# Performance work log

Hardware: AMD Instinct MI355X
Metric: run time of the kernel (lower is better)

The kernel has to match this reference:

```python
import jax, jax.numpy as jnp
import numpy as np
import math

B, N, CS, CZ, H, C, P, PV, NB = 1, 512, 384, 128, 12, 16, 4, 8, 64


def quat_to_rot(q):
    q = q / jnp.clip(jnp.linalg.norm(q, axis=-1, keepdims=True), 1e-8)
    w, x, y, z = q[..., 0], q[..., 1], q[..., 2], q[..., 3]
    return jnp.stack([
        w*w + x*x - y*y - z*z, 2*(x*y - w*z), 2*(x*z + w*y),
        2*(x*y + w*z), w*w - x*x + y*y - z*z, 2*(y*z - w*x),
        2*(x*z - w*y), 2*(y*z + w*x), w*w - x*x - y*y + z*z,
    ], axis=-1).reshape(q.shape[:-1] + (3, 3))


def setup_inputs() -> dict:
    key = jax.random.key(0)
    ks = jax.random.split(key, 28)
    def n(k, shape, sc=1.0):
        return jax.random.normal(k, shape, jnp.float32) * sc
    s = n(ks[0], (B, N, CS))
    z = n(ks[1], (B, N, N, CZ))
    translations = n(ks[2], (B, N, 3)) * 4.0  # spread distances over 0-32A bins
    rotations = quat_to_rot(n(ks[3], (B, N, 4)))  # valid SO(3) frames
    mask = jnp.ones((B, N), dtype=bool)
    inv = lambda fan: 1.0 / math.sqrt(fan)
    return {
        's': s, 'z': z, 'translations': translations, 'rotations': rotations, 'mask': mask,
        'Wq': n(ks[4], (CS, H*C), inv(CS)), 'bq': n(ks[5], (H*C,), 0.01),
        'Wk': n(ks[6], (CS, H*C), inv(CS)), 'bk': n(ks[7], (H*C,), 0.01),
        'Wv': n(ks[8], (CS, H*C), inv(CS)), 'bv': n(ks[9], (H*C,), 0.01),
        'Wqp': n(ks[10], (CS, H*P*3), inv(CS)), 'bqp': n(ks[11], (H*P*3,), 0.01),
        'Wkp': n(ks[12], (CS, H*P*3), inv(CS)), 'bkp': n(ks[13], (H*P*3,), 0.01),
        'Wvp': n(ks[14], (CS, H*PV*3), inv(CS)), 'bvp': n(ks[15], (H*PV*3,), 0.01),
        'Wb': n(ks[16], (CZ, H), inv(CZ)), 'bb': n(ks[17], (H,), 0.01),
        'dist_emb': n(ks[18], (NB, H), 0.02),
        'scale_logits': n(ks[19], (3, H), 0.1),
        'head_weights': jnp.abs(n(ks[20], (H,))) * 0.2 + 0.8,
        'Wout': n(ks[21], (H*(C + PV*4 + CZ), CS), inv(H*(C + PV*4 + CZ))),
        'bout': n(ks[22], (CS,), 0.01),
    }


def reference(s, z, translations, rotations, mask, Wq, bq, Wk, bk, Wv, bv,
              Wqp, bqp, Wkp, bkp, Wvp, bvp, Wb, bb, dist_emb, scale_logits,
              head_weights, Wout, bout):
    b, n, _ = s.shape
    q = (s @ Wq + bq).reshape(b, n, H, C)
    k = (s @ Wk + bk).reshape(b, n, H, C)
    v = (s @ Wv + bv).reshape(b, n, H, C)
    q_pts = (s @ Wqp + bqp).reshape(b, n, H, P, 3)
    k_pts = (s @ Wkp + bkp).reshape(b, n, H, P, 3)
    v_pts = (s @ Wvp + bvp).reshape(b, n, H, PV, 3)
    t = translations[:, :, None, None, :]
    q_g = jnp.einsum('bnij,bnhpj->bnhpi', rotations, q_pts) + t
    k_g = jnp.einsum('bnij,bnhpj->bnhpi', rotations, k_pts) + t
    v_g = jnp.einsum('bnij,bnhpj->bnhpi', rotations, v_pts) + t
    scalar_logits = jnp.einsum('bnhc,bmhc->bnmh', q, k) / math.sqrt(C)
    # squared point distances, summed over points p and coords i, via expansion
    q_sq = (q_g**2).sum((-1, -2))  # (b, n, h)
    k_sq = (k_g**2).sum((-1, -2))
    cross = jnp.einsum('bnhpi,bmhpi->bnmh', q_g, k_g)
    point_dist = q_sq[:, :, None, :] + k_sq[:, None, :, :] - 2.0 * cross
    point_logits = -0.5 * point_dist * head_weights
    pair_bias = z @ Wb + bb  # (b, n, m, h)
    pair_dist = jnp.linalg.norm(
        translations[:, :, None, :] - translations[:, None, :, :], axis=-1)
    edges = jnp.linspace(0.0, 32.0, NB + 1)
    bins = jnp.clip(jnp.searchsorted(edges, pair_dist, side='left') - 1, 0, NB - 1)
    dist_bias = dist_emb[bins]
    local = (pair_dist <= 5.0).astype(s.dtype)
    medium = ((pair_dist > 5.0) & (pair_dist <= 15.0)).astype(s.dtype)
    scales = jnp.stack([local, medium, jnp.ones_like(pair_dist)], axis=-1)
    per_head = jax.nn.softmax(scale_logits, axis=0)  # (3, h)
    multiscale = jnp.einsum('bnms,sh->bnmh', scales, per_head)
    logits = scalar_logits + point_logits + pair_bias + dist_bias + multiscale
    m2d = mask[:, :, None] & mask[:, None, :]
    logits = jnp.where(m2d[..., None], logits, -10000.0)
    attn = jax.nn.softmax(logits.astype(jnp.float32), axis=2).astype(s.dtype)
    out_scalar = jnp.einsum('bnmh,bmhc->bnhc', attn, v)
    out_pts_g = jnp.einsum('bnmh,bmhpi->bnhpi', attn, v_g)
    out_pts_l = jnp.einsum('bnji,bnhpj->bnhpi', rotations, out_pts_g - t)  # R^T x
    out_norms = jnp.linalg.norm(out_pts_l, axis=-1)  # (b, n, h, pv)
    pair_feat = jnp.einsum('bnmh,bnmc->bnhc', attn, z)
    feats = jnp.concatenate(
        [out_scalar, out_pts_l.reshape(b, n, H, PV * 3), out_norms, pair_feat],
        axis=-1).reshape(b, n, -1)
    return feats @ Wout + bout
```

## Files before the change

### kernel.cpp

```cpp
#include <hip/hip_runtime.h>
#include <math.h>

#define N   512
#define CS  384
#define CZ  128
#define H   12
#define C   16
#define P   4
#define PV  8
#define NB  64
#define KSP 528
#define QKD 28
#define QPAD 68
#define APAD 516

#define OFF_Q    0
#define OFF_K    98304
#define OFF_V    196608
#define OFF_QP   294912
#define OFF_KP   368640
#define OFF_VP   442368
#define OFF_QG   589824
#define OFF_KG   663552
#define OFF_VG   737280
#define OFF_QSQ  884736
#define OFF_KSQ  890880
#define OFF_LOG  897024
#define OFF_FEAT 4042752

__global__ __launch_bounds__(256) void k_proj(
    const float* __restrict__ s,
    const float* __restrict__ Wq,  const float* __restrict__ bq,
    const float* __restrict__ Wk,  const float* __restrict__ bk,
    const float* __restrict__ Wv,  const float* __restrict__ bv,
    const float* __restrict__ Wqp, const float* __restrict__ bqp,
    const float* __restrict__ Wkp, const float* __restrict__ bkp,
    const float* __restrict__ Wvp, const float* __restrict__ bvp,
    float* __restrict__ ws)
{
    __shared__ float s_s[16*388];
    __shared__ float part[4*16*68];
    const int tid = threadIdx.x;
    const int n0  = blockIdx.y * 16;
    const int cq  = tid & 15;
    const int rg  = (tid >> 4) & 3;
    const int ks  = tid >> 6;
    const int gc  = blockIdx.x * 64 + cq * 4;
    for (int i = tid; i < 16*384; i += 256) {
        int r = i / 384, c = i - r*384;
        s_s[r*388 + c] = s[(n0 + r)*384 + c];
    }
    __syncthreads();
    const float* W; int width; int lc;
    if      (gc < 192) { W=Wq;  width=192; lc=gc;     }
    else if (gc < 384) { W=Wk;  width=192; lc=gc-192; }
    else if (gc < 576) { W=Wv;  width=192; lc=gc-384; }
    else if (gc < 720) { W=Wqp; width=144; lc=gc-576; }
    else if (gc < 864) { W=Wkp; width=144; lc=gc-720; }
    else               { W=Wvp; width=288; lc=gc-864; }
    float acc[4][4] = {{0.f}};
    const float* wp   = W + lc + (size_t)(ks*96)*width;
    const float* srow = s_s + (rg*4)*388 + ks*96;
    #pragma unroll 4
    for (int kk = 0; kk < 96; kk++) {
        float4 w4 = *(const float4*)(wp + (size_t)kk*width);
        #pragma unroll
        for (int r = 0; r < 4; r++) {
            float sv = srow[r*388 + kk];
            acc[r][0] += sv*w4.x; acc[r][1] += sv*w4.y;
            acc[r][2] += sv*w4.z; acc[r][3] += sv*w4.w;
        }
    }
    #pragma unroll
    for (int r = 0; r < 4; r++)
        *(float4*)(part + (ks*16 + rg*4 + r)*68 + cq*4) =
            make_float4(acc[r][0], acc[r][1], acc[r][2], acc[r][3]);
    __syncthreads();
    {
        const int row = tid >> 4;
        float4 sum = *(const float4*)(part + (0*16 + row)*68 + cq*4);
        #pragma unroll
        for (int k2 = 1; k2 < 4; k2++) {
            float4 p = *(const float4*)(part + (k2*16 + row)*68 + cq*4);
            sum.x += p.x; sum.y += p.y; sum.z += p.z; sum.w += p.w;
        }
        const float* b; float* dst; int w2, lc2;
        if      (gc < 192) { b=bq;  w2=192; lc2=gc;     dst=ws+OFF_Q;  }
        else if (gc < 384) { b=bk;  w2=192; lc2=gc-192; dst=ws+OFF_K;  }
        else if (gc < 576) { b=bv;  w2=192; lc2=gc-384; dst=ws+OFF_V;  }
        else if (gc < 720) { b=bqp; w2=144; lc2=gc-576; dst=ws+OFF_QP; }
        else if (gc < 864) { b=bkp; w2=144; lc2=gc-720; dst=ws+OFF_KP; }
        else               { b=bvp; w2=288; lc2=gc-864; dst=ws+OFF_VP; }
        float4 b4 = *(const float4*)(b + lc2);
        sum.x += b4.x; sum.y += b4.y; sum.z += b4.z; sum.w += b4.w;
        *(float4*)(dst + (size_t)(n0+row)*w2 + lc2) = sum;
    }
}

__global__ __launch_bounds__(192) void k_frames(
    const float* __restrict__ rot, const float* __restrict__ trans,
    float* __restrict__ ws)
{
    int n = blockIdx.x, tid = threadIdx.x;
    __shared__ float R[9], T[3], qg_s[144], kg_s[144];
    if (tid < 9) R[tid] = rot[n*9 + tid];
    if (tid < 3) T[tid] = trans[n*3 + tid];
    __syncthreads();
    if (tid < 48) {
        const float* lp = ws + OFF_QP + n*144 + tid*3;
        float l0=lp[0], l1=lp[1], l2=lp[2];
        float* gp = ws + OFF_QG + n*144 + tid*3;
        for (int i=0;i<3;i++){ float g = R[i*3+0]*l0 + R[i*3+1]*l1 + R[i*3+2]*l2 + T[i]; gp[i]=g; qg_s[tid*3+i]=g; }
    } else if (tid < 96) {
        int u = tid-48;
        const float* lp = ws + OFF_KP + n*144 + u*3;
        float l0=lp[0], l1=lp[1], l2=lp[2];
        float* gp = ws + OFF_KG + n*144 + u*3;
        for (int i=0;i<3;i++){ float g = R[i*3+0]*l0 + R[i*3+1]*l1 + R[i*3+2]*l2 + T[i]; gp[i]=g; kg_s[u*3+i]=g; }
    } else {
        int u = tid-96;
        const float* lp = ws + OFF_VP + n*288 + u*3;
        float l0=lp[0], l1=lp[1], l2=lp[2];
        float* gp = ws + OFF_VG + n*288 + u*3;
        for (int i=0;i<3;i++){ float g = R[i*3+0]*l0 + R[i*3+1]*l1 + R[i*3+2]*l2 + T[i]; gp[i]=g; }
    }
    __syncthreads();
    if (tid < 12) {
        float a=0;
        for (int d=0; d<12; d++){ float x=qg_s[tid*12+d]; a+=x*x; }
        ws[OFF_QSQ + n*12 + tid]=a;
    } else if (tid < 24) {
        int h = tid-12; float a=0;
        for (int d=0; d<12; d++){ float x=kg_s[h*12+d]; a+=x*x; }
        ws[OFF_KSQ + n*12 + h]=a;
    }
}

__global__ __launch_bounds__(256) void k_qkpt(
    const float* __restrict__ head_weights, float* __restrict__ ws)
{
    __shared__ float qs[QKD*QPAD], ks[QKD*QPAD], qa[64], kb[64];
    const int tid = threadIdx.x;
    const int m0 = blockIdx.x * 64, n0 = blockIdx.y * 64, h = blockIdx.z;
    const float hw = head_weights[h];
    for (int idx = tid; idx < 64*16; idx += 256) {
        int r = idx >> 4, c = idx & 15;
        qs[c*QPAD + r] = ws[OFF_Q + (n0+r)*192 + h*16 + c] * 0.25f;
        ks[c*QPAD + r] = ws[OFF_K + (m0+r)*192 + h*16 + c];
    }
    for (int idx = tid; idx < 64*12; idx += 256) {
        int r = idx / 12, c = idx % 12;
        qs[(16+c)*QPAD + r] = ws[OFF_QG + (n0+r)*144 + h*12 + c] * hw;
        ks[(16+c)*QPAD + r] = ws[OFF_KG + (m0+r)*144 + h*12 + c];
    }
    for (int idx = tid; idx < 64; idx += 256) {
        qa[idx] = -0.5f * hw * ws[OFF_QSQ + (n0+idx)*12 + h];
        kb[idx] = -0.5f * hw * ws[OFF_KSQ + (m0+idx)*12 + h];
    }
    __syncthreads();
    const int tx = tid & 15, ty = tid >> 4;
    float acc[4][4] = {{0.f}};
    #pragma unroll 4
    for (int d = 0; d < QKD; d++) {
        float4 a = *(const float4*)(qs + d*QPAD + ty*4);
        float4 b = *(const float4*)(ks + d*QPAD + tx*4);
        const float* ap = &a.x; const float* bp = &b.x;
        #pragma unroll
        for (int i=0;i<4;i++)
            #pragma unroll
            for (int j=0;j<4;j++) acc[i][j] += ap[i]*bp[j];
    }
    #pragma unroll
    for (int i=0;i<4;i++) {
        float ai = qa[ty*4+i];
        float4 r;
        r.x = acc[i][0] + ai + kb[tx*4+0];
        r.y = acc[i][1] + ai + kb[tx*4+1];
        r.z = acc[i][2] + ai + kb[tx*4+2];
        r.w = acc[i][3] + ai + kb[tx*4+3];
        *(float4*)(ws + OFF_LOG + ((size_t)(n0+ty*4+i)*H + h)*N + m0 + tx*4) = r;
    }
}

__global__ __launch_bounds__(256) void k_attn_all(
    const float* __restrict__ z, const float* __restrict__ trans,
    const float* __restrict__ rot,
    const float* __restrict__ Wb, const float* __restrict__ bb,
    const float* __restrict__ dist_emb, const float* __restrict__ scale_logits,
    float* __restrict__ ws)
{
    __shared__ float attn_s[H*APAD];
    __shared__ float part[4*12*64];
    __shared__ float og_s[288];
    const int n = blockIdx.x, tid = threadIdx.x;
    const int lane = tid & 63, wave = tid >> 6;

    const float4* asrc = (const float4*)(ws + OFF_LOG + (size_t)n*H*N);
    for (int i = tid; i < H*(N/4); i += 256) {
        int h = i >> 7, q = i & 127;
        *(float4*)(attn_s + h*APAD + q*4) = asrc[h*128 + q];
    }
    __syncthreads();

    const float tnx = trans[n*3+0], tny = trans[n*3+1], tnz = trans[n*3+2];
    for (int half = 0; half < 2; half++) {
        const int m = tid + half*256;
        float dx = tnx - trans[m*3+0];
        float dy = tny - trans[m*3+1];
        float dz = tnz - trans[m*3+2];
        float pd = sqrtf(dx*dx+dy*dy+dz*dz);
        int bin = (int)ceilf(2.f*pd) - 1;
        bin = bin < 0 ? 0 : (bin > NB-1 ? NB-1 : bin);
        const float4 de0 = *(const float4*)(dist_emb + bin*12);
        const float4 de1 = *(const float4*)(dist_emb + bin*12 + 4);
        const float4 de2 = *(const float4*)(dist_emb + bin*12 + 8);
        float de[12] = {de0.x,de0.y,de0.z,de0.w, de1.x,de1.y,de1.z,de1.w, de2.x,de2.y,de2.z,de2.w};
        float acc[12];
        #pragma unroll
        for (int h=0; h<12; h++) {
            float sa = scale_logits[0*H+h], sb = scale_logits[1*H+h], sc = scale_logits[2*H+h];
            float mx = fmaxf(sa, fmaxf(sb,sc));
            float ea=__expf(sa-mx), eb=__expf(sb-mx), ec=__expf(sc-mx);
            float inv = 1.f/(ea+eb+ec);
            float msc = ec*inv;
            if (pd <= 5.f)       msc += ea*inv;
            else if (pd <= 15.f) msc += eb*inv;
            acc[h] = bb[h] + de[h] + msc;
        }
        const float* zp = z + ((size_t)n*N + m)*CZ;
        #pragma unroll 2
        for (int c4 = 0; c4 < CZ/4; c4++) {
            float4 z4 = *(const float4*)(zp + c4*4);
            const float* zv = &z4.x;
            #pragma unroll
            for (int j=0; j<4; j++)
                #pragma unroll
                for (int h=0; h<12; h++)
                    acc[h] += zv[j] * Wb[(c4*4+j)*H + h];
        }
        #pragma unroll
        for (int h=0; h<12; h++)
            attn_s[h*APAD + m] += acc[h];
    }
    __syncthreads();

    for (int h = wave; h < H; h += 4) {
        float* row = attn_s + h*APAD;
        float v[8]; float mx = -1e30f;
        #pragma unroll
        for (int j=0;j<8;j++){ v[j]=row[lane + j*64]; mx = fmaxf(mx, v[j]); }
        #pragma unroll
        for (int off=32; off>0; off>>=1) mx = fmaxf(mx, __shfl_xor(mx, off, 64));
        float sum = 0.f;
        #pragma unroll
        for (int j=0;j<8;j++){ v[j]=__expf(v[j]-mx); sum += v[j]; }
        #pragma unroll
        for (int off=32; off>0; off>>=1) sum += __shfl_xor(sum, off, 64);
        float inv = 1.f/sum;
        #pragma unroll
        for (int j=0;j<8;j++) row[lane + j*64] = v[j]*inv;
    }
    __syncthreads();

    const int cq = tid & 15;
    const int ms = tid >> 4;
    for (int ch = 0; ch < 2; ch++) {
        const float* zb = z + (size_t)n*N*CZ + ch*64 + cq*4;
        float4 acc[12];
        #pragma unroll
        for (int h=0; h<12; h++) acc[h] = make_float4(0.f,0.f,0.f,0.f);
        const int r0 = ms*32;
        #pragma unroll 2
        for (int rq = 0; rq < 8; rq++) {
            const int r = r0 + rq*4;
            float4 z0 = *(const float4*)(zb + (size_t)(r+0)*CZ);
            float4 z1 = *(const float4*)(zb + (size_t)(r+1)*CZ);
            float4 z2 = *(const float4*)(zb + (size_t)(r+2)*CZ);
            float4 z3 = *(const float4*)(zb + (size_t)(r+3)*CZ);
            #pragma unroll
            for (int h=0; h<12; h++) {
                float4 a4 = *(const float4*)(attn_s + h*APAD + r);
                acc[h].x += a4.x*z0.x + a4.y*z1.x + a4.z*z2.x + a4.w*z3.x;
                acc[h].y += a4.x*z0.y + a4.y*z1.y + a4.z*z2.y + a4.w*z3.y;
                acc[h].z += a4.x*z0.z + a4.y*z1.z + a4.z*z2.z + a4.w*z3.z;
                acc[h].w += a4.x*z0.w + a4.y*z1.w + a4.z*z2.w + a4.w*z3.w;
            }
        }
        #pragma unroll
        for (int h=0; h<12; h++) {
            acc[h].x += __shfl_xor(acc[h].x, 16, 64); acc[h].y += __shfl_xor(acc[h].y, 16, 64);
            acc[h].z += __shfl_xor(acc[h].z, 16, 64); acc[h].w += __shfl_xor(acc[h].w, 16, 64);
            acc[h].x += __shfl_xor(acc[h].x, 32, 64); acc[h].y += __shfl_xor(acc[h].y, 32, 64);
            acc[h].z += __shfl_xor(acc[h].z, 32, 64); acc[h].w += __shfl_xor(acc[h].w, 32, 64);
        }
        if (lane < 16) {
            #pragma unroll
            for (int h=0; h<12; h++)
                *(float4*)(part + (wave*12 + h)*64 + lane*4) = acc[h];
        }
        __syncthreads();
        if (tid < 192) {
            const int h = tid >> 4, c4 = tid & 15;
            float4 s4 = *(const float4*)(part + (0*12 + h)*64 + c4*4);
            #pragma unroll
            for (int w=1; w<4; w++) {
                float4 p = *(const float4*)(part + (w*12 + h)*64 + c4*4);
                s4.x += p.x; s4.y += p.y; s4.z += p.z; s4.w += p.w;
            }
            *(float4*)(ws + OFF_FEAT + (size_t)n*2112 + h*176 + 48 + ch*64 + c4*4) = s4;
        }
        __syncthreads();
    }

    if (tid < 240) {
        const int col4 = (tid % 120) * 4;
        const int msA  = tid / 120;
        const float* aptr; int astride, ah;
        if (col4 < 192) { ah = col4 >> 4;        aptr = ws + OFF_V  + col4;       astride = 192; }
        else            { ah = (col4-192) / 24;  aptr = ws + OFF_VG + (col4-192); astride = 288; }
        const float4* arow = (const float4*)(attn_s + ah*APAD);
        float4 acc = {0.f,0.f,0.f,0.f};
        #pragma unroll 2
        for (int mq = msA*64; mq < msA*64 + 64; mq++) {
            float4 a4 = arow[mq];
            const float* vp = aptr + (size_t)mq*4*astride;
            float4 v0 = *(const float4*)(vp);
            float4 v1 = *(const float4*)(vp + astride);
            float4 v2 = *(const float4*)(vp + 2*astride);
            float4 v3 = *(const float4*)(vp + 3*astride);
            acc.x += a4.x*v0.x + a4.y*v1.x + a4.z*v2.x + a4.w*v3.x;
            acc.y += a4.x*v0.y + a4.y*v1.y + a4.z*v2.y + a4.w*v3.y;
            acc.z += a4.x*v0.z + a4.y*v1.z + a4.z*v2.z + a4.w*v3.z;
            acc.w += a4.x*v0.w + a4.y*v1.w + a4.z*v2.w + a4.w*v3.w;
        }
        *(float4*)(part + tid*4) = acc;
    }
    __syncthreads();
    if (tid < 120) {
        const int col4 = tid * 4;
        float4 a = *(const float4*)(part + tid*4);
        float4 b = *(const float4*)(part + (tid+120)*4);
        a.x += b.x; a.y += b.y; a.z += b.z; a.w += b.w;
        if (col4 < 192) {
            const int ah = col4 >> 4;
            *(float4*)(ws + OFF_FEAT + (size_t)n*2112 + ah*176 + (col4 & 15)) = a;
        } else {
            *(float4*)(og_s + (col4 - 192)) = a;
        }
    }
    __syncthreads();
    if (tid < 96) {
        const int h = tid >> 3, p = tid & 7;
        float g0 = og_s[h*24 + p*3 + 0] - trans[n*3+0];
        float g1 = og_s[h*24 + p*3 + 1] - trans[n*3+1];
        float g2 = og_s[h*24 + p*3 + 2] - trans[n*3+2];
        const float* R = rot + n*9;
        float* fdst = ws + OFF_FEAT + (size_t)n*2112 + h*176;
        float nsq = 0.f;
        #pragma unroll
        for (int i=0;i<3;i++){
            float l = R[0*3+i]*g0 + R[1*3+i]*g1 + R[2*3+i]*g2;
            fdst[16 + p*3 + i] = l;
            nsq += l*l;
        }
        fdst[40 + p] = sqrtf(nsq);
    }
}

__global__ __launch_bounds__(384) void k_bias(
    const float* __restrict__ bout, float* __restrict__ out)
{
    out[(size_t)blockIdx.x*CS + threadIdx.x] = bout[threadIdx.x];
}

__global__ __launch_bounds__(256) void k_out(
    const float* __restrict__ Wout, const float* __restrict__ ws,
    float* __restrict__ out)
{
    __shared__ float f_s[16*KSP];
    __shared__ float part[4*16*68];
    const int tid = threadIdx.x;
    const int n0  = blockIdx.y * 16;
    const int k0  = blockIdx.z * KSP;
    const int cq  = tid & 15;
    const int rg  = (tid >> 4) & 3;
    const int ks  = tid >> 6;
    const int col = blockIdx.x * 64 + cq * 4;
    for (int i = tid; i < 16*KSP; i += 256) {
        int r = i / KSP, c = i - r*KSP;
        f_s[i] = ws[OFF_FEAT + (size_t)(n0 + r)*2112 + k0 + c];
    }
    __syncthreads();
    float acc[4][4] = {{0.f}};
    const float* wp = Wout + (size_t)(k0 + ks*132)*CS + col;
    const float* f0 = f_s + (rg*4)*KSP + ks*132;
    #pragma unroll 4
    for (int kk = 0; kk < 132; kk++) {
        float4 w4 = *(const float4*)(wp + (size_t)kk*CS);
        #pragma unroll
        for (int r = 0; r < 4; r++) {
            float fv = f0[r*KSP + kk];
            acc[r][0] += fv*w4.x; acc[r][1] += fv*w4.y;
            acc[r][2] += fv*w4.z; acc[r][3] += fv*w4.w;
        }
    }
    #pragma unroll
    for (int r = 0; r < 4; r++)
        *(float4*)(part + (ks*16 + rg*4 + r)*68 + cq*4) =
            make_float4(acc[r][0], acc[r][1], acc[r][2], acc[r][3]);
    __syncthreads();
    {
        const int row = tid >> 4;
        float4 s = *(const float4*)(part + (0*16 + row)*68 + cq*4);
        #pragma unroll
        for (int k2 = 1; k2 < 4; k2++) {
            float4 p = *(const float4*)(part + (k2*16 + row)*68 + cq*4);
            s.x += p.x; s.y += p.y; s.z += p.z; s.w += p.w;
        }
        float* o = out + (size_t)(n0+row)*CS + col;
        atomicAdd(o+0, s.x); atomicAdd(o+1, s.y);
        atomicAdd(o+2, s.z); atomicAdd(o+3, s.w);
    }
}

extern "C" void kernel_launch(void* const* d_in, const int* in_sizes, int n_in,
                              void* d_out, int out_size, void* d_ws, size_t ws_size,
                              hipStream_t stream) {
    const float* s     = (const float*)d_in[0];
    const float* z     = (const float*)d_in[1];
    const float* trans = (const float*)d_in[2];
    const float* rot   = (const float*)d_in[3];
    const float* Wq  = (const float*)d_in[5];  const float* bq  = (const float*)d_in[6];
    const float* Wk  = (const float*)d_in[7];  const float* bk  = (const float*)d_in[8];
    const float* Wv  = (const float*)d_in[9];  const float* bv  = (const float*)d_in[10];
    const float* Wqp = (const float*)d_in[11]; const float* bqp = (const float*)d_in[12];
    const float* Wkp = (const float*)d_in[13]; const float* bkp = (const float*)d_in[14];
    const float* Wvp = (const float*)d_in[15]; const float* bvp = (const float*)d_in[16];
    const float* Wb  = (const float*)d_in[17]; const float* bb  = (const float*)d_in[18];
    const float* dist_emb     = (const float*)d_in[19];
    const float* scale_logits = (const float*)d_in[20];
    const float* head_weights = (const float*)d_in[21];
    const float* Wout = (const float*)d_in[22]; const float* bout = (const float*)d_in[23];
    float* out = (float*)d_out;
    float* ws  = (float*)d_ws;

    k_proj<<<dim3(18, 32), 256, 0, stream>>>(s, Wq,bq, Wk,bk, Wv,bv, Wqp,bqp, Wkp,bkp, Wvp,bvp, ws);
    k_frames<<<N, 192, 0, stream>>>(rot, trans, ws);
    k_qkpt<<<dim3(8, 8, 12), 256, 0, stream>>>(head_weights, ws);
    k_attn_all<<<N, 256, 0, stream>>>(z, trans, rot, Wb, bb, dist_emb, scale_logits, ws);
    k_bias<<<N, CS, 0, stream>>>(bout, out);
    k_out<<<dim3(6, 32, 4), 256, 0, stream>>>(Wout, ws, out);
}
```

Before: 344.2 us.

## Restructure attention kernel loops for more memory-level parallelism and hoisted softmax

Precomputes the per-head scale softmax once per block into shared memory instead of per thread per head. It processes both m halves of the pair-bias pass at once with vectorized Wb loads, and runs both 64-channel halves of the z aggregation in a single pass. The attn·V loop gains a double-buffered register prefetch of value rows. A launch bound of two blocks per CU is added. These aim to hide global-memory latency with more loads in flight, at the cost of much higher register pressure, which the launch bound may force into spills.

```diff
diff --git a/kernel.cpp b/kernel.cpp
--- a/kernel.cpp
+++ b/kernel.cpp
@@ -182,7 +182,7 @@
     }
 }
 
-__global__ __launch_bounds__(256) void k_attn_all(
+__global__ __launch_bounds__(256, 2) void k_attn_all(
     const float* __restrict__ z, const float* __restrict__ trans,
     const float* __restrict__ rot,
     const float* __restrict__ Wb, const float* __restrict__ bb,
@@ -192,8 +192,17 @@
     __shared__ float attn_s[H*APAD];
     __shared__ float part[4*12*64];
     __shared__ float og_s[288];
+    __shared__ float sprob[36];
     const int n = blockIdx.x, tid = threadIdx.x;
     const int lane = tid & 63, wave = tid >> 6;
+
+    if (tid < 12) {
+        float sa = scale_logits[tid], sb = scale_logits[12+tid], sc = scale_logits[24+tid];
+        float mx = fmaxf(sa, fmaxf(sb, sc));
+        float ea=__expf(sa-mx), eb=__expf(sb-mx), ec=__expf(sc-mx);
+        float inv = 1.f/(ea+eb+ec);
+        sprob[tid] = ea*inv; sprob[12+tid] = eb*inv; sprob[24+tid] = ec*inv;
+    }
 
     const float4* asrc = (const float4*)(ws + OFF_LOG + (size_t)n*H*N);
     for (int i = tid; i < H*(N/4); i += 256) {
@@ -202,45 +211,88 @@
     }
     __syncthreads();
 
-    const float tnx = trans[n*3+0], tny = trans[n*3+1], tnz = trans[n*3+2];
-    for (int half = 0; half < 2; half++) {
-        const int m = tid + half*256;
-        float dx = tnx - trans[m*3+0];
-        float dy = tny - trans[m*3+1];
-        float dz = tnz - trans[m*3+2];
-        float pd = sqrtf(dx*dx+dy*dy+dz*dz);
-        int bin = (int)ceilf(2.f*pd) - 1;
-        bin = bin < 0 ? 0 : (bin > NB-1 ? NB-1 : bin);
-        const float4 de0 = *(const float4*)(dist_emb + bin*12);
-        const float4 de1 = *(const float4*)(dist_emb + bin*12 + 4);
-        const float4 de2 = *(const float4*)(dist_emb + bin*12 + 8);
-        float de[12] = {de0.x,de0.y,de0.z,de0.w, de1.x,de1.y,de1.z,de1.w, de2.x,de2.y,de2.z,de2.w};
-        float acc[12];
-        #pragma unroll
-        for (int h=0; h<12; h++) {
-            float sa = scale_logits[0*H+h], sb = scale_logits[1*H+h], sc = scale_logits[2*H+h];
-            float mx = fmaxf(sa, fmaxf(sb,sc));
-            float ea=__expf(sa-mx), eb=__expf(sb-mx), ec=__expf(sc-mx);
-            float inv = 1.f/(ea+eb+ec);
-            float msc = ec*inv;
-            if (pd <= 5.f)       msc += ea*inv;
-            else if (pd <= 15.f) msc += eb*inv;
-            acc[h] = bb[h] + de[h] + msc;
-        }
-        const float* zp = z + ((size_t)n*N + m)*CZ;
+    {
+        const int mA = tid, mB = tid + 256;
+        const float tnx = trans[n*3+0], tny = trans[n*3+1], tnz = trans[n*3+2];
+        float dxA = tnx - trans[mA*3+0], dyA = tny - trans[mA*3+1], dzA = tnz - trans[mA*3+2];
+        float dxB = tnx - trans[mB*3+0], dyB = tny - trans[mB*3+1], dzB = tnz - trans[mB*3+2];
+        float pdA = sqrtf(dxA*dxA+dyA*dyA+dzA*dzA);
+        float pdB = sqrtf(dxB*dxB+dyB*dyB+dzB*dzB);
+        int binA = (int)ceilf(2.f*pdA) - 1; binA = binA < 0 ? 0 : (binA > NB-1 ? NB-1 : binA);
+        int binB = (int)ceilf(2.f*pdB) - 1; binB = binB < 0 ? 0 : (binB > NB-1 ? NB-1 : binB);
+        const float4 bb0 = *(const float4*)(bb);
+        const float4 bb1 = *(const float4*)(bb+4);
+        const float4 bb2 = *(const float4*)(bb+8);
+        const float4 pc0 = *(const float4*)(sprob+24);
+        const float4 pc1 = *(const float4*)(sprob+28);
+        const float4 pc2 = *(const float4*)(sprob+32);
+        float4 aA0, aA1, aA2, aB0, aB1, aB2;
+        {
+            float4 de0 = *(const float4*)(dist_emb + binA*12);
+            float4 de1 = *(const float4*)(dist_emb + binA*12 + 4);
+            float4 de2 = *(const float4*)(dist_emb + binA*12 + 8);
+            aA0.x = bb0.x+de0.x+pc0.x; aA0.y = bb0.y+de0.y+pc0.y; aA0.z = bb0.z+de0.z+pc0.z; aA0.w = bb0.w+de0.w+pc0.w;
+            aA1.x = bb1.x+de1.x+pc1.x; aA1.y = bb1.y+de1.y+pc1.y; aA1.z = bb1.z+de1.z+pc1.z; aA1.w = bb1.w+de1.w+pc1.w;
+            aA2.x = bb2.x+de2.x+pc2.x; aA2.y = bb2.y+de2.y+pc2.y; aA2.z = bb2.z+de2.z+pc2.z; aA2.w = bb2.w+de2.w+pc2.w;
+            const int sselA = (pdA <= 5.f) ? 0 : (pdA <= 15.f ? 1 : -1);
+            if (sselA >= 0) {
+                const float* sp = sprob + sselA*12;
+                float4 p0 = *(const float4*)(sp), p1 = *(const float4*)(sp+4), p2 = *(const float4*)(sp+8);
+                aA0.x += p0.x; aA0.y += p0.y; aA0.z += p0.z; aA0.w += p0.w;
+                aA1.x += p1.x; aA1.y += p1.y; aA1.z += p1.z; aA1.w += p1.w;
+                aA2.x += p2.x; aA2.y += p2.y; aA2.z += p2.z; aA2.w += p2.w;
+            }
+        }
+        {
+            float4 de0 = *(const float4*)(dist_emb + binB*12);
+            float4 de1 = *(const float4*)(dist_emb + binB*12 + 4);
+            float4 de2 = *(const float4*)(dist_emb + binB*12 + 8);
+            aB0.x = bb0.x+de0.x+pc0.x; aB0.y = bb0.y+de0.y+pc0.y; aB0.z = bb0.z+de0.z+pc0.z; aB0.w = bb0.w+de0.w+pc0.w;
+            aB1.x = bb1.x+de1.x+pc1.x; aB1.y = bb1.y+de1.y+pc1.y; aB1.z = bb1.z+de1.z+pc1.z; aB1.w = bb1.w+de1.w+pc1.w;
+            aB2.x = bb2.x+de2.x+pc2.x; aB2.y = bb2.y+de2.y+pc2.y; aB2.z = bb2.z+de2.z+pc2.z; aB2.w = bb2.w+de2.w+pc2.w;
+            const int sselB = (pdB <= 5.f) ? 0 : (pdB <= 15.f ? 1 : -1);
+            if (sselB >= 0) {
+                const float* sp = sprob + sselB*12;
+                float4 p0 = *(const float4*)(sp), p1 = *(const float4*)(sp+4), p2 = *(const float4*)(sp+8);
+                aB0.x += p0.x; aB0.y += p0.y; aB0.z += p0.z; aB0.w += p0.w;
+                aB1.x += p1.x; aB1.y += p1.y; aB1.z += p1.z; aB1.w += p1.w;
+                aB2.x += p2.x; aB2.y += p2.y; aB2.z += p2.z; aB2.w += p2.w;
+            }
+        }
+        const float* zpA = z + ((size_t)n*N + mA)*CZ;
+        const float* zpB = zpA + (size_t)256*CZ;
         #pragma unroll 2
         for (int c4 = 0; c4 < CZ/4; c4++) {
-            float4 z4 = *(const float4*)(zp + c4*4);
-            const float* zv = &z4.x;
-            #pragma unroll
-            for (int j=0; j<4; j++)
-                #pragma unroll
-                for (int h=0; h<12; h++)
-                    acc[h] += zv[j] * Wb[(c4*4+j)*H + h];
-        }
-        #pragma unroll
-        for (int h=0; h<12; h++)
-            attn_s[h*APAD + m] += acc[h];
+            float4 zA = *(const float4*)(zpA + c4*4);
+            float4 zB = *(const float4*)(zpB + c4*4);
+            const float* zav = &zA.x; const float* zbv = &zB.x;
+            #pragma unroll
+            for (int j=0; j<4; j++) {
+                const float* wr = Wb + (c4*4+j)*12;
+                float4 w0 = *(const float4*)(wr);
+                float4 w1 = *(const float4*)(wr+4);
+                float4 w2 = *(const float4*)(wr+8);
+                float za = zav[j], zb2 = zbv[j];
+                aA0.x += za*w0.x; aA0.y += za*w0.y; aA0.z += za*w0.z; aA0.w += za*w0.w;
+                aA1.x += za*w1.x; aA1.y += za*w1.y; aA1.z += za*w1.z; aA1.w += za*w1.w;
+                aA2.x += za*w2.x; aA2.y += za*w2.y; aA2.z += za*w2.z; aA2.w += za*w2.w;
+                aB0.x += zb2*w0.x; aB0.y += zb2*w0.y; aB0.z += zb2*w0.z; aB0.w += zb2*w0.w;
+                aB1.x += zb2*w1.x; aB1.y += zb2*w1.y; aB1.z += zb2*w1.z; aB1.w += zb2*w1.w;
+                aB2.x += zb2*w2.x; aB2.y += zb2*w2.y; aB2.z += zb2*w2.z; aB2.w += zb2*w2.w;
+            }
+        }
+        attn_s[0*APAD + mA] += aA0.x;  attn_s[1*APAD + mA] += aA0.y;
+        attn_s[2*APAD + mA] += aA0.z;  attn_s[3*APAD + mA] += aA0.w;
+        attn_s[4*APAD + mA] += aA1.x;  attn_s[5*APAD + mA] += aA1.y;
+        attn_s[6*APAD + mA] += aA1.z;  attn_s[7*APAD + mA] += aA1.w;
+        attn_s[8*APAD + mA] += aA2.x;  attn_s[9*APAD + mA] += aA2.y;
+        attn_s[10*APAD + mA] += aA2.z; attn_s[11*APAD + mA] += aA2.w;
+        attn_s[0*APAD + mB] += aB0.x;  attn_s[1*APAD + mB] += aB0.y;
+        attn_s[2*APAD + mB] += aB0.z;  attn_s[3*APAD + mB] += aB0.w;
+        attn_s[4*APAD + mB] += aB1.x;  attn_s[5*APAD + mB] += aB1.y;
+        attn_s[6*APAD + mB] += aB1.z;  attn_s[7*APAD + mB] += aB1.w;
+        attn_s[8*APAD + mB] += aB2.x;  attn_s[9*APAD + mB] += aB2.y;
+        attn_s[10*APAD + mB] += aB2.z; attn_s[11*APAD + mB] += aB2.w;
     }
     __syncthreads();
 
@@ -264,39 +316,48 @@
 
     const int cq = tid & 15;
     const int ms = tid >> 4;
-    for (int ch = 0; ch < 2; ch++) {
-        const float* zb = z + (size_t)n*N*CZ + ch*64 + cq*4;
-        float4 acc[12];
-        #pragma unroll
-        for (int h=0; h<12; h++) acc[h] = make_float4(0.f,0.f,0.f,0.f);
+    {
+        const float* zb0 = z + (size_t)n*N*CZ + cq*4;
+        const float* zb1 = zb0 + 64;
+        float4 acc0[12], acc1[12];
+        #pragma unroll
+        for (int h=0; h<12; h++) { acc0[h] = make_float4(0.f,0.f,0.f,0.f); acc1[h] = acc0[h]; }
         const int r0 = ms*32;
         #pragma unroll 2
         for (int rq = 0; rq < 8; rq++) {
             const int r = r0 + rq*4;
-            float4 z0 = *(const float4*)(zb + (size_t)(r+0)*CZ);
-            float4 z1 = *(const float4*)(zb + (size_t)(r+1)*CZ);
-            float4 z2 = *(const float4*)(zb + (size_t)(r+2)*CZ);
-            float4 z3 = *(const float4*)(zb + (size_t)(r+3)*CZ);
+            float4 p0 = *(const float4*)(zb0 + (size_t)(r+0)*CZ);
+            float4 p1 = *(const float4*)(zb0 + (size_t)(r+1)*CZ);
+            float4 p2 = *(const float4*)(zb0 + (size_t)(r+2)*CZ);
+            float4 p3 = *(const float4*)(zb0 + (size_t)(r+3)*CZ);
+            float4 q0 = *(const float4*)(zb1 + (size_t)(r+0)*CZ);
+            float4 q1 = *(const float4*)(zb1 + (size_t)(r+1)*CZ);
+            float4 q2 = *(const float4*)(zb1 + (size_t)(r+2)*CZ);
+            float4 q3 = *(const float4*)(zb1 + (size_t)(r+3)*CZ);
             #pragma unroll
             for (int h=0; h<12; h++) {
                 float4 a4 = *(const float4*)(attn_s + h*APAD + r);
-                acc[h].x += a4.x*z0.x + a4.y*z1.x + a4.z*z2.x + a4.w*z3.x;
-                acc[h].y += a4.x*z0.y + a4.y*z1.y + a4.z*z2.y + a4.w*z3.y;
-                acc[h].z += a4.x*z0.z + a4.y*z1.z + a4.z*z2.z + a4.w*z3.z;
-                acc[h].w += a4.x*z0.w + a4.y*z1.w + a4.z*z2.w + a4.w*z3.w;
+                acc0[h].x += a4.x*p0.x + a4.y*p1.x + a4.z*p2.x + a4.w*p3.x;
+                acc0[h].y += a4.x*p0.y + a4.y*p1.y + a4.z*p2.y + a4.w*p3.y;
+                acc0[h].z += a4.x*p0.z + a4.y*p1.z + a4.z*p2.z + a4.w*p3.z;
+                acc0[h].w += a4.x*p0.w + a4.y*p1.w + a4.z*p2.w + a4.w*p3.w;
+                acc1[h].x += a4.x*q0.x + a4.y*q1.x + a4.z*q2.x + a4.w*q3.x;
+                acc1[h].y += a4.x*q0.y + a4.y*q1.y + a4.z*q2.y + a4.w*q3.y;
+                acc1[h].z += a4.x*q0.z + a4.y*q1.z + a4.z*q2.z + a4.w*q3.z;
+                acc1[h].w += a4.x*q0.w + a4.y*q1.w + a4.z*q2.w + a4.w*q3.w;
             }
         }
         #pragma unroll
         for (int h=0; h<12; h++) {
-            acc[h].x += __shfl_xor(acc[h].x, 16, 64); acc[h].y += __shfl_xor(acc[h].y, 16, 64);
-            acc[h].z += __shfl_xor(acc[h].z, 16, 64); acc[h].w += __shfl_xor(acc[h].w, 16, 64);
-            acc[h].x += __shfl_xor(acc[h].x, 32, 64); acc[h].y += __shfl_xor(acc[h].y, 32, 64);
-            acc[h].z += __shfl_xor(acc[h].z, 32, 64); acc[h].w += __shfl_xor(acc[h].w, 32, 64);
+            acc0[h].x += __shfl_xor(acc0[h].x, 16, 64); acc0[h].y += __shfl_xor(acc0[h].y, 16, 64);
+            acc0[h].z += __shfl_xor(acc0[h].z, 16, 64); acc0[h].w += __shfl_xor(acc0[h].w, 16, 64);
+            acc0[h].x += __shfl_xor(acc0[h].x, 32, 64); acc0[h].y += __shfl_xor(acc0[h].y, 32, 64);
+            acc0[h].z += __shfl_xor(acc0[h].z, 32, 64); acc0[h].w += __shfl_xor(acc0[h].w, 32, 64);
         }
         if (lane < 16) {
             #pragma unroll
             for (int h=0; h<12; h++)
-                *(float4*)(part + (wave*12 + h)*64 + lane*4) = acc[h];
+                *(float4*)(part + (wave*12 + h)*64 + lane*4) = acc0[h];
         }
         __syncthreads();
         if (tid < 192) {
@@ -307,7 +368,31 @@
                 float4 p = *(const float4*)(part + (w*12 + h)*64 + c4*4);
                 s4.x += p.x; s4.y += p.y; s4.z += p.z; s4.w += p.w;
             }
-            *(float4*)(ws + OFF_FEAT + (size_t)n*2112 + h*176 + 48 + ch*64 + c4*4) = s4;
+            *(float4*)(ws + OFF_FEAT + (size_t)n*2112 + h*176 + 48 + c4*4) = s4;
+        }
+        __syncthreads();
+        #pragma unroll
+        for (int h=0; h<12; h++) {
+            acc1[h].x += __shfl_xor(acc1[h].x, 16, 64); acc1[h].y += __shfl_xor(acc1[h].y, 16, 64);
+            acc1[h].z += __shfl_xor(acc1[h].z, 16, 64); acc1[h].w += __shfl_xor(acc1[h].w, 16, 64);
+            acc1[h].x += __shfl_xor(acc1[h].x, 32, 64); acc1[h].y += __shfl_xor(acc1[h].y, 32, 64);
+            acc1[h].z += __shfl_xor(acc1[h].z, 32, 64); acc1[h].w += __shfl_xor(acc1[h].w, 32, 64);
+        }
+        if (lane < 16) {
+            #pragma unroll
+            for (int h=0; h<12; h++)
+                *(float4*)(part + (wave*12 + h)*64 + lane*4) = acc1[h];
+        }
+        __syncthreads();
+        if (tid < 192) {
+            const int h = tid >> 4, c4 = tid & 15;
+            float4 s4 = *(const float4*)(part + (0*12 + h)*64 + c4*4);
+            #pragma unroll
+            for (int w=1; w<4; w++) {
+                float4 p = *(const float4*)(part + (w*12 + h)*64 + c4*4);
+                s4.x += p.x; s4.y += p.y; s4.z += p.z; s4.w += p.w;
+            }
+            *(float4*)(ws + OFF_FEAT + (size_t)n*2112 + h*176 + 48 + 64 + c4*4) = s4;
         }
         __syncthreads();
     }
@@ -319,19 +404,37 @@
         if (col4 < 192) { ah = col4 >> 4;        aptr = ws + OFF_V  + col4;       astride = 192; }
         else            { ah = (col4-192) / 24;  aptr = ws + OFF_VG + (col4-192); astride = 288; }
         const float4* arow = (const float4*)(attn_s + ah*APAD);
+        const int rbase = msA*256;
+        const int qbase = msA*64;
         float4 acc = {0.f,0.f,0.f,0.f};
-        #pragma unroll 2
-        for (int mq = msA*64; mq < msA*64 + 64; mq++) {
-            float4 a4 = arow[mq];
-            const float* vp = aptr + (size_t)mq*4*astride;
-            float4 v0 = *(const float4*)(vp);
-            float4 v1 = *(const float4*)(vp + astride);
-            float4 v2 = *(const float4*)(vp + 2*astride);
-            float4 v3 = *(const float4*)(vp + 3*astride);
-            acc.x += a4.x*v0.x + a4.y*v1.x + a4.z*v2.x + a4.w*v3.x;
-            acc.y += a4.x*v0.y + a4.y*v1.y + a4.z*v2.y + a4.w*v3.y;
-            acc.z += a4.x*v0.z + a4.y*v1.z + a4.z*v2.z + a4.w*v3.z;
-            acc.w += a4.x*v0.w + a4.y*v1.w + a4.z*v2.w + a4.w*v3.w;
+        float4 bA[16], bB[16];
+        #pragma unroll
+        for (int r=0;r<16;r++) bA[r] = *(const float4*)(aptr + (size_t)(rbase + r)*astride);
+        #pragma unroll 1
+        for (int g2 = 0; g2 < 8; g2++) {
+            const int gA = g2*2, gB = g2*2+1;
+            #pragma unroll
+            for (int r=0;r<16;r++) bB[r] = *(const float4*)(aptr + (size_t)(rbase + gB*16 + r)*astride);
+            #pragma unroll
+            for (int q=0;q<4;q++) {
+                float4 a4 = arow[qbase + gA*4 + q];
+                acc.x += a4.x*bA[q*4+0].x + a4.y*bA[q*4+1].x + a4.z*bA[q*4+2].x + a4.w*bA[q*4+3].x;
+                acc.y += a4.x*bA[q*4+0].y + a4.y*bA[q*4+1].y + a4.z*bA[q*4+2].y + a4.w*bA[q*4+3].y;
+                acc.z += a4.x*bA[q*4+0].z + a4.y*bA[q*4+1].z + a4.z*bA[q*4+2].z + a4.w*bA[q*4+3].z;
+                acc.w += a4.x*bA[q*4+0].w + a4.y*bA[q*4+1].w + a4.z*bA[q*4+2].w + a4.w*bA[q*4+3].w;
+            }
+            if (g2 < 7) {
+                #pragma unroll
+                for (int r=0;r<16;r++) bA[r] = *(const float4*)(aptr + (size_t)(rbase + (gA+2)*16 + r)*astride);
+            }
+            #pragma unroll
+            for (int q=0;q<4;q++) {
+                float4 a4 = arow[qbase + gB*4 + q];
+                acc.x += a4.x*bB[q*4+0].x + a4.y*bB[q*4+1].x + a4.z*bB[q*4+2].x + a4.w*bB[q*4+3].x;
+                acc.y += a4.x*bB[q*4+0].y + a4.y*bB[q*4+1].y + a4.z*bB[q*4+2].y + a4.w*bB[q*4+3].y;
+                acc.z += a4.x*bB[q*4+0].z + a4.y*bB[q*4+1].z + a4.z*bB[q*4+2].z + a4.w*bB[q*4+3].z;
+                acc.w += a4.x*bB[q*4+0].w + a4.y*bB[q*4+1].w + a4.z*bB[q*4+2].w + a4.w*bB[q*4+3].w;
+            }
         }
         *(float4*)(part + tid*4) = acc;
     }
```

Result: slower. 363.1 us (+5.5%).

## Stage z rows in shared memory and split pair-bias channels across waves

Applied to the files above, without the earlier changes.

The pair-bias projection in the attention kernel now loads 64-row chunks of z cooperatively into padded LDS with coalesced float4 loads. Each wave projects a 32-channel slice against Wb cached in shared memory, and the partial sums are reduced through LDS. Before this, every thread streamed its own 512-byte z row with strided global loads and read Wb from global memory. The scale-logit softmax is also computed once per block instead of per element. The change adds three barriers per chunk and more shared memory, which may reduce occupancy.

```diff
diff --git a/kernel.cpp b/kernel.cpp
--- a/kernel.cpp
+++ b/kernel.cpp
@@ -13,6 +13,7 @@
 #define QKD 28
 #define QPAD 68
 #define APAD 516
+#define ZPAD 132
 
 #define OFF_Q    0
 #define OFF_K    98304
@@ -190,10 +191,24 @@
     float* __restrict__ ws)
 {
     __shared__ float attn_s[H*APAD];
-    __shared__ float part[4*12*64];
+    __shared__ float zs[64*ZPAD];
+    __shared__ float partial[4*64*13];
+    __shared__ float Wb_s[CZ*12];
     __shared__ float og_s[288];
+    __shared__ float sprob[36];
+    float* part = zs;
     const int n = blockIdx.x, tid = threadIdx.x;
     const int lane = tid & 63, wave = tid >> 6;
+
+    if (tid < 12) {
+        float sa = scale_logits[tid], sb = scale_logits[12+tid], sc = scale_logits[24+tid];
+        float mx = fmaxf(sa, fmaxf(sb, sc));
+        float ea=__expf(sa-mx), eb=__expf(sb-mx), ec=__expf(sc-mx);
+        float inv = 1.f/(ea+eb+ec);
+        sprob[tid] = ea*inv; sprob[12+tid] = eb*inv; sprob[24+tid] = ec*inv;
+    }
+    for (int i = tid; i < 384; i += 256)
+        *(float4*)(Wb_s + i*4) = *(const float4*)(Wb + i*4);
 
     const float4* asrc = (const float4*)(ws + OFF_LOG + (size_t)n*H*N);
     for (int i = tid; i < H*(N/4); i += 256) {
@@ -202,47 +217,75 @@
     }
     __syncthreads();
 
-    const float tnx = trans[n*3+0], tny = trans[n*3+1], tnz = trans[n*3+2];
-    for (int half = 0; half < 2; half++) {
-        const int m = tid + half*256;
-        float dx = tnx - trans[m*3+0];
-        float dy = tny - trans[m*3+1];
-        float dz = tnz - trans[m*3+2];
-        float pd = sqrtf(dx*dx+dy*dy+dz*dz);
-        int bin = (int)ceilf(2.f*pd) - 1;
-        bin = bin < 0 ? 0 : (bin > NB-1 ? NB-1 : bin);
-        const float4 de0 = *(const float4*)(dist_emb + bin*12);
-        const float4 de1 = *(const float4*)(dist_emb + bin*12 + 4);
-        const float4 de2 = *(const float4*)(dist_emb + bin*12 + 8);
-        float de[12] = {de0.x,de0.y,de0.z,de0.w, de1.x,de1.y,de1.z,de1.w, de2.x,de2.y,de2.z,de2.w};
-        float acc[12];
-        #pragma unroll
-        for (int h=0; h<12; h++) {
-            float sa = scale_logits[0*H+h], sb = scale_logits[1*H+h], sc = scale_logits[2*H+h];
-            float mx = fmaxf(sa, fmaxf(sb,sc));
-            float ea=__expf(sa-mx), eb=__expf(sb-mx), ec=__expf(sc-mx);
-            float inv = 1.f/(ea+eb+ec);
-            float msc = ec*inv;
-            if (pd <= 5.f)       msc += ea*inv;
-            else if (pd <= 15.f) msc += eb*inv;
-            acc[h] = bb[h] + de[h] + msc;
-        }
-        const float* zp = z + ((size_t)n*N + m)*CZ;
-        #pragma unroll 2
-        for (int c4 = 0; c4 < CZ/4; c4++) {
-            float4 z4 = *(const float4*)(zp + c4*4);
-            const float* zv = &z4.x;
+    {
+        const float tnx = trans[n*3+0], tny = trans[n*3+1], tnz = trans[n*3+2];
+        const int h0 = wave*3;
+        const float bbv0 = bb[h0], bbv1 = bb[h0+1], bbv2 = bb[h0+2];
+        const float spc0 = sprob[24+h0], spc1 = sprob[24+h0+1], spc2 = sprob[24+h0+2];
+        const float spa0 = sprob[h0],    spa1 = sprob[h0+1],    spa2 = sprob[h0+2];
+        const float spb0 = sprob[12+h0], spb1 = sprob[12+h0+1], spb2 = sprob[12+h0+2];
+        const float4* zsrc4 = (const float4*)(z + (size_t)n*N*CZ);
+        for (int chunk = 0; chunk < 8; chunk++) {
             #pragma unroll
-            for (int j=0; j<4; j++)
+            for (int pass = 0; pass < 8; pass++) {
+                int idx = pass*256 + tid;
+                float4 v = zsrc4[chunk*2048 + idx];
+                *(float4*)(zs + (idx>>5)*ZPAD + (idx&31)*4) = v;
+            }
+            __syncthreads();
+            {
+                const float* zrow = zs + lane*ZPAD + wave*32;
+                float a[12];
                 #pragma unroll
-                for (int h=0; h<12; h++)
-                    acc[h] += zv[j] * Wb[(c4*4+j)*H + h];
-        }
-        #pragma unroll
-        for (int h=0; h<12; h++)
-            attn_s[h*APAD + m] += acc[h];
-    }
-    __syncthreads();
+                for (int h=0;h<12;h++) a[h]=0.f;
+                #pragma unroll
+                for (int c4=0;c4<8;c4++) {
+                    float4 zq = *(const float4*)(zrow + c4*4);
+                    const float* wr = Wb_s + (wave*32 + c4*4)*12;
+                    const float* zp = &zq.x;
+                    #pragma unroll
+                    for (int j=0;j<4;j++) {
+                        float4 w0 = *(const float4*)(wr + j*12);
+                        float4 w1 = *(const float4*)(wr + j*12 + 4);
+                        float4 w2 = *(const float4*)(wr + j*12 + 8);
+                        float zj = zp[j];
+                        a[0]+=zj*w0.x; a[1]+=zj*w0.y; a[2]+=zj*w0.z; a[3]+=zj*w0.w;
+                        a[4]+=zj*w1.x; a[5]+=zj*w1.y; a[6]+=zj*w1.z; a[7]+=zj*w1.w;
+                        a[8]+=zj*w2.x; a[9]+=zj*w2.y; a[10]+=zj*w2.z; a[11]+=zj*w2.w;
+                    }
+                }
+                float* pdst = partial + (wave*64 + lane)*13;
+                #pragma unroll
+                for (int h=0;h<12;h++) pdst[h] = a[h];
+            }
+            __syncthreads();
+            {
+                const int m = chunk*64 + lane;
+                float dx = tnx - trans[m*3+0];
+                float dy = tny - trans[m*3+1];
+                float dz = tnz - trans[m*3+2];
+                float pdist = sqrtf(dx*dx+dy*dy+dz*dz);
+                int bin = (int)ceilf(2.f*pdist) - 1;
+                bin = bin < 0 ? 0 : (bin > NB-1 ? NB-1 : bin);
+                const int ssel = (pdist <= 5.f) ? 0 : (pdist <= 15.f ? 1 : -1);
+                float v0 = partial[(0*64+lane)*13 + h0]   + partial[(1*64+lane)*13 + h0]
+                         + partial[(2*64+lane)*13 + h0]   + partial[(3*64+lane)*13 + h0];
+                float v1 = partial[(0*64+lane)*13 + h0+1] + partial[(1*64+lane)*13 + h0+1]
+                         + partial[(2*64+lane)*13 + h0+1] + partial[(3*64+lane)*13 + h0+1];
+                float v2 = partial[(0*64+lane)*13 + h0+2] + partial[(1*64+lane)*13 + h0+2]
+                         + partial[(2*64+lane)*13 + h0+2] + partial[(3*64+lane)*13 + h0+2];
+                v0 += bbv0 + dist_emb[bin*12 + h0]   + spc0;
+                v1 += bbv1 + dist_emb[bin*12 + h0+1] + spc1;
+                v2 += bbv2 + dist_emb[bin*12 + h0+2] + spc2;
+                if (ssel == 0)      { v0 += spa0; v1 += spa1; v2 += spa2; }
+                else if (ssel == 1) { v0 += spb0; v1 += spb1; v2 += spb2; }
+                attn_s[(h0  )*APAD + m] += v0;
+                attn_s[(h0+1)*APAD + m] += v1;
+                attn_s[(h0+2)*APAD + m] += v2;
+            }
+            __syncthreads();
+        }
+    }
 
     for (int h = wave; h < H; h += 4) {
         float* row = attn_s + h*APAD;
```

Result: slower. 364.9 us (+6.0%).
